# Kernel tuning notes

Measured on AMD Instinct MI355X. Metric: run time of the kernel, lower is better.

The kernel has to match this reference:

```python
import jax, jax.numpy as jnp
import numpy as np

B, S, D, H = 2, 2048, 1024, 16
DEPTH = D // H


def setup_inputs() -> dict:
    key = jax.random.key(0)
    ks = jax.random.split(key, 13)
    std = 1.0 / np.sqrt(D)
    inp = {
        'q': jax.random.normal(ks[0], (B, S, D), jnp.float32),
        'k': jax.random.normal(ks[1], (B, S, D), jnp.float32),
        'v': jax.random.normal(ks[2], (B, S, D), jnp.float32),
        # padding-style mask broadcastable to [B,H,Sq,Sk]; 1 = masked
        'mask': (jax.random.uniform(ks[3], (B, 1, 1, S)) < 0.1).astype(jnp.float32),
        'wq_w': jax.random.uniform(ks[4], (D, D), jnp.float32, -std, std),
        'wq_b': jax.random.uniform(ks[5], (D,), jnp.float32, -std, std),
        'wk_w': jax.random.uniform(ks[6], (D, D), jnp.float32, -std, std),
        'wk_b': jax.random.uniform(ks[7], (D,), jnp.float32, -std, std),
        'wv_w': jax.random.uniform(ks[8], (D, D), jnp.float32, -std, std),
        'wv_b': jax.random.uniform(ks[9], (D,), jnp.float32, -std, std),
        'wo_w': jax.random.uniform(ks[10], (D, D), jnp.float32, -std, std),
        'wo_b': jax.random.uniform(ks[11], (D,), jnp.float32, -std, std),
    }
    return inp


def _split_heads(x):
    # [B,S,D] -> [B,H,S,depth]
    b, s, _ = x.shape
    return x.reshape(b, s, H, DEPTH).transpose(0, 2, 1, 3)


def reference(q, k, v, mask, wq_w, wq_b, wk_w, wk_b, wv_w, wv_b, wo_w, wo_b):
    qh = _split_heads(q @ wq_w.T + wq_b)
    kh = _split_heads(k @ wk_w.T + wk_b)
    vh = _split_heads(v @ wv_w.T + wv_b)
    scale = 1.0 / jnp.sqrt(jnp.float32(DEPTH))
    logits = jnp.einsum('bhqd,bhkd->bhqk', qh, kh) * scale  # [B,H,S,S]
    logits = logits + mask * (-1e9)
    weights = jax.nn.softmax(logits, axis=-1)
    attn = jnp.einsum('bhqk,bhkd->bhqd', weights, vh)
    concat = attn.transpose(0, 2, 1, 3).reshape(q.shape[0], -1, D)
    out = concat @ wo_w.T + wo_b
    return out, weights
```

## Files before the change

### kernel.cpp

```cpp
#include <hip/hip_runtime.h>
#include <stdint.h>
#include <stddef.h>

static constexpr int NB = 2;
static constexpr int SS = 2048;
static constexpr int DDim = 1024;
static constexpr int NH = 16;
static constexpr size_t BSD = (size_t)NB * SS * DDim;
static constexpr size_t DDn = (size_t)DDim * DDim;

typedef __attribute__((ext_vector_type(4))) float f32x4;
typedef __attribute__((ext_vector_type(8))) short bf16x8;

__device__ __forceinline__ short f2bf(float f) {
  union { float f; unsigned u; } v; v.f = f;
  unsigned r = v.u + 0x7FFFu + ((v.u >> 16) & 1u);
  return (short)(r >> 16);
}

__device__ __forceinline__ void gload_lds16(const void* src, void* dst) {
  __builtin_amdgcn_global_load_lds(
      (const __attribute__((address_space(1))) void*)src,
      (__attribute__((address_space(3))) void*)dst, 16, 0, 0);
}

__global__ void cvt_k(const float* __restrict__ in, short* __restrict__ out, int n8) {
  int i = blockIdx.x * 256 + threadIdx.x;
  if (i >= n8) return;
  const f32x4* p = (const f32x4*)in + (size_t)i * 2;
  f32x4 a = p[0], c = p[1];
  bf16x8 o;
  o[0] = f2bf(a[0]); o[1] = f2bf(a[1]); o[2] = f2bf(a[2]); o[3] = f2bf(a[3]);
  o[4] = f2bf(c[0]); o[5] = f2bf(c[1]); o[6] = f2bf(c[2]); o[7] = f2bf(c[3]);
  ((bf16x8*)out)[i] = o;
}

__device__ __forceinline__ void gemm_core(
    const short* __restrict__ A, const short* __restrict__ Bm,
    int rowA, int rowB, int ld, int nk,
    short* la, short* lb, int wid, int lane, f32x4 (&acc)[4][4]) {
  const int ar = lane & 15, ak = (lane >> 4) * 8;
  const int srow = lane >> 2, scol = (lane & 3) * 8;
  const int wr = wid >> 1, wc = wid & 1;
  for (int kt = 0; kt < nk; ++kt) {
    const int k0 = kt * 32;
#pragma unroll
    for (int c = 0; c < 2; ++c) {
      int chunk = c * 4 + wid;
      gload_lds16(A + (size_t)(rowA + chunk * 16 + srow) * ld + k0 + scol, la + chunk * 512);
      gload_lds16(Bm + (size_t)(rowB + chunk * 16 + srow) * ld + k0 + scol, lb + chunk * 512);
    }
    asm volatile("s_waitcnt vmcnt(0)" ::: "memory");
    __syncthreads();
    bf16x8 af[4], bfr[4];
#pragma unroll
    for (int m = 0; m < 4; ++m)
      af[m] = *(const bf16x8*)(la + (wr * 64 + m * 16 + ar) * 32 + ak);
#pragma unroll
    for (int n = 0; n < 4; ++n)
      bfr[n] = *(const bf16x8*)(lb + (wc * 64 + n * 16 + ar) * 32 + ak);
#pragma unroll
    for (int m = 0; m < 4; ++m)
#pragma unroll
      for (int n = 0; n < 4; ++n)
        acc[m][n] = __builtin_amdgcn_mfma_f32_16x16x32_bf16(af[m], bfr[n], acc[m][n], 0, 0, 0);
    __syncthreads();
  }
}

template <int MODE>
__global__ __launch_bounds__(256, 2) void gemm128(
    const short* __restrict__ A, const short* __restrict__ Bm,
    const float* __restrict__ bias, void* __restrict__ outp, int N, int ld, int nk) {
  __shared__ short la[128 * 32], lb[128 * 32];
  const int tid = threadIdx.x, wid = tid >> 6, lane = tid & 63;
  const int bM = blockIdx.y * 128, bN = blockIdx.x * 128;
  f32x4 acc[4][4];
#pragma unroll
  for (int m = 0; m < 4; ++m)
#pragma unroll
    for (int n = 0; n < 4; ++n) acc[m][n] = (f32x4){0.f, 0.f, 0.f, 0.f};
  gemm_core(A, Bm, bM, bN, ld, nk, la, lb, wid, lane, acc);
  const int wr = wid >> 1, wc = wid & 1;
#pragma unroll
  for (int m = 0; m < 4; ++m)
#pragma unroll
    for (int n = 0; n < 4; ++n)
#pragma unroll
      for (int r = 0; r < 4; ++r) {
        int gm = bM + wr * 64 + m * 16 + (lane >> 4) * 4 + r;
        int gn = bN + wc * 64 + n * 16 + (lane & 15);
        float val = acc[m][n][r] + bias[gn];
        if constexpr (MODE == 0) {
          int b = gm >> 11, s = gm & 2047, h = gn >> 6, d = gn & 63;
          ((short*)outp)[(((size_t)b * NH + h) * SS + s) * 64 + d] = f2bf(val);
        } else if constexpr (MODE == 1) {
          int b = gm >> 11, s = gm & 2047, h = gn >> 6, d = gn & 63;
          ((short*)outp)[(((size_t)b * NH + h) * 64 + d) * SS + s] = f2bf(val);
        } else {
          ((float*)outp)[(size_t)gm * N + gn] = val;
        }
      }
}

__global__ __launch_bounds__(256, 2) void attn_k(
    const short* __restrict__ qh, const short* __restrict__ kh,
    const short* __restrict__ vhT, const float* __restrict__ mask,
    float* __restrict__ wout, short* __restrict__ concat) {
  __shared__ short lP[128 * 128];
  __shared__ short lK[128 * 64];
  __shared__ short lV[64 * 128];
  __shared__ float lmask[2048];
  __shared__ float lrs[2][128];
  const int tid = threadIdx.x, wid = tid >> 6, lane = tid & 63;
  const int wr = wid >> 1, wc = wid & 1;
  const int bh = blockIdx.y, b = bh >> 4, h = bh & 15;
  const int bM = blockIdx.x * 128;
  const short* Qb = qh + (size_t)bh * SS * 64 + (size_t)bM * 64;
  const short* Kb = kh + (size_t)bh * SS * 64;
  const short* Vb = vhT + (size_t)bh * 64 * SS;
  float* Wb = wout + (size_t)bh * SS * SS;

#pragma unroll
  for (int i = 0; i < 8; ++i)
    lmask[tid + i * 256] = mask[b * SS + tid + i * 256] * (-1e9f);

#pragma unroll
  for (int c = 0; c < 4; ++c) {
    int ob = c * 4096 + tid * 16;
    int row = ob >> 7, inrow = ob & 127;
    gload_lds16(Qb + row * 64 + ((inrow ^ ((row & 7) << 4)) >> 1), (char*)lP + ob);
  }
  asm volatile("s_waitcnt vmcnt(0)" ::: "memory");
  __syncthreads();
  bf16x8 af[4][2];
#pragma unroll
  for (int m = 0; m < 4; ++m)
#pragma unroll
    for (int kk = 0; kk < 2; ++kk) {
      int row = wr * 64 + m * 16 + (lane & 15);
      int kb = (kk * 32 + (lane >> 4) * 8) * 2;
      af[m][kk] = *(const bf16x8*)((const char*)lP + row * 128 + (kb ^ ((row & 7) << 4)));
    }

  float ps[4][4];
#pragma unroll
  for (int m = 0; m < 4; ++m)
#pragma unroll
    for (int r = 0; r < 4; ++r) ps[m][r] = 0.f;

  for (int kt = 0; kt < 16; ++kt) {
    __syncthreads();
#pragma unroll
    for (int c = 0; c < 4; ++c) {
      int ob = c * 4096 + tid * 16;
      int row = ob >> 7, inrow = ob & 127;
      gload_lds16(Kb + (size_t)(kt * 128 + row) * 64 + ((inrow ^ ((row & 7) << 4)) >> 1),
                  (char*)lK + ob);
    }
    asm volatile("s_waitcnt vmcnt(0)" ::: "memory");
    __syncthreads();
    bf16x8 bfr[4][2];
#pragma unroll
    for (int n = 0; n < 4; ++n)
#pragma unroll
      for (int kk = 0; kk < 2; ++kk) {
        int row = wc * 64 + n * 16 + (lane & 15);
        int kb = (kk * 32 + (lane >> 4) * 8) * 2;
        bfr[n][kk] = *(const bf16x8*)((const char*)lK + row * 128 + (kb ^ ((row & 7) << 4)));
      }
#pragma unroll
    for (int n = 0; n < 4; ++n) {
      float mv = lmask[kt * 128 + wc * 64 + n * 16 + (lane & 15)];
#pragma unroll
      for (int m = 0; m < 4; ++m) {
        f32x4 a = (f32x4){0.f, 0.f, 0.f, 0.f};
        a = __builtin_amdgcn_mfma_f32_16x16x32_bf16(af[m][0], bfr[n][0], a, 0, 0, 0);
        a = __builtin_amdgcn_mfma_f32_16x16x32_bf16(af[m][1], bfr[n][1], a, 0, 0, 0);
#pragma unroll
        for (int r = 0; r < 4; ++r) ps[m][r] += __expf(a[r] * 0.125f + mv);
      }
    }
  }
#pragma unroll
  for (int m = 0; m < 4; ++m)
#pragma unroll
    for (int r = 0; r < 4; ++r) {
      float s = ps[m][r];
      s += __shfl_xor(s, 1, 64);
      s += __shfl_xor(s, 2, 64);
      s += __shfl_xor(s, 4, 64);
      s += __shfl_xor(s, 8, 64);
      ps[m][r] = s;
    }
  if ((lane & 15) == 0) {
#pragma unroll
    for (int m = 0; m < 4; ++m)
#pragma unroll
      for (int r = 0; r < 4; ++r)
        lrs[wc][wr * 64 + m * 16 + (lane >> 4) * 4 + r] = ps[m][r];
  }
  __syncthreads();
  float inv[4][4];
#pragma unroll
  for (int m = 0; m < 4; ++m)
#pragma unroll
    for (int r = 0; r < 4; ++r) {
      int row = wr * 64 + m * 16 + (lane >> 4) * 4 + r;
      inv[m][r] = 1.f / (lrs[0][row] + lrs[1][row]);
    }

  f32x4 pacc[4][2];
#pragma unroll
  for (int m = 0; m < 4; ++m)
#pragma unroll
    for (int n = 0; n < 2; ++n) pacc[m][n] = (f32x4){0.f, 0.f, 0.f, 0.f};

  for (int kt = 0; kt < 16; ++kt) {
    __syncthreads();
#pragma unroll
    for (int c = 0; c < 4; ++c) {
      int ob = c * 4096 + tid * 16;
      int row = ob >> 7, inrow = ob & 127;
      gload_lds16(Kb + (size_t)(kt * 128 + row) * 64 + ((inrow ^ ((row & 7) << 4)) >> 1),
                  (char*)lK + ob);
    }
#pragma unroll
    for (int c = 0; c < 4; ++c) {
      int ob = c * 4096 + tid * 16;
      int row = ob >> 8, inrow = ob & 255;
      gload_lds16(Vb + (size_t)row * SS + kt * 128 + ((inrow ^ ((row & 7) << 4)) >> 1),
                  (char*)lV + ob);
    }
    asm volatile("s_waitcnt vmcnt(0)" ::: "memory");
    __syncthreads();
    bf16x8 bfr[4][2];
#pragma unroll
    for (int n = 0; n < 4; ++n)
#pragma unroll
      for (int kk = 0; kk < 2; ++kk) {
        int row = wc * 64 + n * 16 + (lane & 15);
        int kb = (kk * 32 + (lane >> 4) * 8) * 2;
        bfr[n][kk] = *(const bf16x8*)((const char*)lK + row * 128 + (kb ^ ((row & 7) << 4)));
      }
#pragma unroll
    for (int n = 0; n < 4; ++n) {
      int col = wc * 64 + n * 16 + (lane & 15);
      float mv = lmask[kt * 128 + col];
#pragma unroll
      for (int m = 0; m < 4; ++m) {
        f32x4 a = (f32x4){0.f, 0.f, 0.f, 0.f};
        a = __builtin_amdgcn_mfma_f32_16x16x32_bf16(af[m][0], bfr[n][0], a, 0, 0, 0);
        a = __builtin_amdgcn_mfma_f32_16x16x32_bf16(af[m][1], bfr[n][1], a, 0, 0, 0);
#pragma unroll
        for (int r = 0; r < 4; ++r) {
          int prow = wr * 64 + m * 16 + (lane >> 4) * 4 + r;
          float w = __expf(a[r] * 0.125f + mv) * inv[m][r];
          Wb[(size_t)(bM + prow) * SS + kt * 128 + col] = w;
          *(short*)((char*)lP + prow * 256 + ((col * 2) ^ ((prow & 7) << 4))) = f2bf(w);
        }
      }
    }
    __syncthreads();
#pragma unroll
    for (int kk = 0; kk < 4; ++kk) {
      bf16x8 pa[4], bv[2];
      int kb = (kk * 32 + (lane >> 4) * 8) * 2;
#pragma unroll
      for (int m = 0; m < 4; ++m) {
        int row = wr * 64 + m * 16 + (lane & 15);
        pa[m] = *(const bf16x8*)((const char*)lP + row * 256 + (kb ^ ((row & 7) << 4)));
      }
#pragma unroll
      for (int n = 0; n < 2; ++n) {
        int d = wc * 32 + n * 16 + (lane & 15);
        bv[n] = *(const bf16x8*)((const char*)lV + d * 256 + (kb ^ ((d & 7) << 4)));
      }
#pragma unroll
      for (int m = 0; m < 4; ++m)
#pragma unroll
        for (int n = 0; n < 2; ++n)
          pacc[m][n] = __builtin_amdgcn_mfma_f32_16x16x32_bf16(pa[m], bv[n], pacc[m][n], 0, 0, 0);
    }
  }
#pragma unroll
  for (int m = 0; m < 4; ++m)
#pragma unroll
    for (int n = 0; n < 2; ++n)
#pragma unroll
      for (int r = 0; r < 4; ++r) {
        int s = bM + wr * 64 + m * 16 + (lane >> 4) * 4 + r;
        int d = wc * 32 + n * 16 + (lane & 15);
        concat[((size_t)(b * SS + s)) * DDim + h * 64 + d] = f2bf(pacc[m][n][r]);
      }
}

extern "C" void kernel_launch(void* const* d_in, const int* in_sizes, int n_in,
                              void* d_out, int out_size, void* d_ws, size_t ws_size,
                              hipStream_t stream) {
  const float* q = (const float*)d_in[0];
  const float* k = (const float*)d_in[1];
  const float* v = (const float*)d_in[2];
  const float* mask = (const float*)d_in[3];
  const float* wq_w = (const float*)d_in[4];
  const float* wq_b = (const float*)d_in[5];
  const float* wk_w = (const float*)d_in[6];
  const float* wk_b = (const float*)d_in[7];
  const float* wv_w = (const float*)d_in[8];
  const float* wv_b = (const float*)d_in[9];
  const float* wo_w = (const float*)d_in[10];
  const float* wo_b = (const float*)d_in[11];

  short* qb = (short*)d_ws;
  short* kb = qb + BSD;
  short* vb = kb + BSD;
  short* wqb = vb + BSD;
  short* wkb = wqb + DDn;
  short* wvb = wkb + DDn;
  short* wob = wvb + DDn;
  short* qh = wob + DDn;
  short* kh = qh + BSD;
  short* vhT = kh + BSD;
  short* concat = vhT + BSD;

  float* out0 = (float*)d_out;
  float* wts = out0 + BSD;

  const int n8_bsd = (int)(BSD / 8), n8_dd = (int)(DDn / 8);
  cvt_k<<<n8_bsd / 256, 256, 0, stream>>>(q, qb, n8_bsd);
  cvt_k<<<n8_bsd / 256, 256, 0, stream>>>(k, kb, n8_bsd);
  cvt_k<<<n8_bsd / 256, 256, 0, stream>>>(v, vb, n8_bsd);
  cvt_k<<<n8_dd / 256, 256, 0, stream>>>(wq_w, wqb, n8_dd);
  cvt_k<<<n8_dd / 256, 256, 0, stream>>>(wk_w, wkb, n8_dd);
  cvt_k<<<n8_dd / 256, 256, 0, stream>>>(wv_w, wvb, n8_dd);
  cvt_k<<<n8_dd / 256, 256, 0, stream>>>(wo_w, wob, n8_dd);

  dim3 gproj(DDim / 128, (NB * SS) / 128);
  gemm128<0><<<gproj, 256, 0, stream>>>(qb, wqb, wq_b, qh, DDim, DDim, DDim / 32);
  gemm128<0><<<gproj, 256, 0, stream>>>(kb, wkb, wk_b, kh, DDim, DDim, DDim / 32);
  gemm128<1><<<gproj, 256, 0, stream>>>(vb, wvb, wv_b, vhT, DDim, DDim, DDim / 32);

  dim3 gattn(SS / 128, NB * NH);
  attn_k<<<gattn, 256, 0, stream>>>(qh, kh, vhT, mask, wts, concat);

  gemm128<2><<<gproj, 256, 0, stream>>>(concat, wob, wo_b, (void*)out0, DDim, DDim, DDim / 32);
}
```

Before: 331.4 us.

## Batch conversions and QKV projections into fewer launches with double-buffered GEMM

Merges the seven fp32-to-bf16 conversion launches into two and the three Q/K/V projection GEMMs into one launch with a z-dimension over projections. The GEMM main loop now double-buffers LDS tiles, so the next k-tile is issued before the current one's MFMAs and only one barrier is needed per iteration. The attention softmax switches from __expf to exp2f, with the log2(e) factor folded into the scale and mask constants. These changes target launch overhead, small-grid tail effects and load latency, at the cost of twice the LDS per GEMM block.

Result: faster. 315.5 us (-4.8%).

```diff
diff --git a/kernel.cpp b/kernel.cpp
--- a/kernel.cpp
+++ b/kernel.cpp
@@ -12,6 +12,9 @@
 typedef __attribute__((ext_vector_type(4))) float f32x4;
 typedef __attribute__((ext_vector_type(8))) short bf16x8;
 
+static constexpr float SCL2 = 0.125f * 1.4426950408889634f;
+static constexpr float MSK2 = -1.4426950408889634e9f;
+
 __device__ __forceinline__ short f2bf(float f) {
   union { float f; unsigned u; } v; v.f = f;
   unsigned r = v.u + 0x7FFFu + ((v.u >> 16) & 1u);
@@ -24,10 +27,13 @@
       (__attribute__((address_space(3))) void*)dst, 16, 0, 0);
 }
 
-__global__ void cvt_k(const float* __restrict__ in, short* __restrict__ out, int n8) {
+__global__ void cvtw_k(const float* __restrict__ w0, const float* __restrict__ w1,
+                       const float* __restrict__ w2, const float* __restrict__ w3,
+                       short* __restrict__ out) {
   int i = blockIdx.x * 256 + threadIdx.x;
-  if (i >= n8) return;
-  const f32x4* p = (const f32x4*)in + (size_t)i * 2;
+  int mat = i >> 17;
+  const float* src = mat == 0 ? w0 : mat == 1 ? w1 : mat == 2 ? w2 : w3;
+  const f32x4* p = (const f32x4*)src + (size_t)(i & 131071) * 2;
   f32x4 a = p[0], c = p[1];
   bf16x8 o;
   o[0] = f2bf(a[0]); o[1] = f2bf(a[1]); o[2] = f2bf(a[2]); o[3] = f2bf(a[3]);
@@ -35,53 +41,70 @@
   ((bf16x8*)out)[i] = o;
 }
 
-__device__ __forceinline__ void gemm_core(
-    const short* __restrict__ A, const short* __restrict__ Bm,
-    int rowA, int rowB, int ld, int nk,
-    short* la, short* lb, int wid, int lane, f32x4 (&acc)[4][4]) {
+__global__ void cvt3_k(const float* __restrict__ t0, const float* __restrict__ t1,
+                       const float* __restrict__ t2, short* __restrict__ out) {
+  int i = blockIdx.x * 256 + threadIdx.x;
+  int mat = i >> 19;
+  const float* src = mat == 0 ? t0 : mat == 1 ? t1 : t2;
+  const f32x4* p = (const f32x4*)src + (size_t)(i & 524287) * 2;
+  f32x4 a = p[0], c = p[1];
+  bf16x8 o;
+  o[0] = f2bf(a[0]); o[1] = f2bf(a[1]); o[2] = f2bf(a[2]); o[3] = f2bf(a[3]);
+  o[4] = f2bf(c[0]); o[5] = f2bf(c[1]); o[6] = f2bf(c[2]); o[7] = f2bf(c[3]);
+  ((bf16x8*)out)[i] = o;
+}
+
+__global__ __launch_bounds__(256, 2) void proj3_k(
+    const short* __restrict__ Acat, const short* __restrict__ Bcat,
+    const float* __restrict__ bq, const float* __restrict__ bk, const float* __restrict__ bv,
+    short* __restrict__ qh, short* __restrict__ kh, short* __restrict__ vhT) {
+  __shared__ short la[2][4096], lb[2][4096];
+  const int tid = threadIdx.x, wid = tid >> 6, lane = tid & 63;
+  const int proj = blockIdx.z;
+  const short* A = Acat + (size_t)proj * BSD;
+  const short* Bm = Bcat + (size_t)proj * DDn;
+  const float* bias = proj == 0 ? bq : proj == 1 ? bk : bv;
+  const int bM = blockIdx.y * 128, bN = blockIdx.x * 128;
   const int ar = lane & 15, ak = (lane >> 4) * 8;
   const int srow = lane >> 2, scol = (lane & 3) * 8;
   const int wr = wid >> 1, wc = wid & 1;
-  for (int kt = 0; kt < nk; ++kt) {
+  f32x4 acc[4][4];
+#pragma unroll
+  for (int m = 0; m < 4; ++m)
+#pragma unroll
+    for (int n = 0; n < 4; ++n) acc[m][n] = (f32x4){0.f, 0.f, 0.f, 0.f};
+
+  auto stage = [&](int kt, int bb) {
     const int k0 = kt * 32;
 #pragma unroll
     for (int c = 0; c < 2; ++c) {
       int chunk = c * 4 + wid;
-      gload_lds16(A + (size_t)(rowA + chunk * 16 + srow) * ld + k0 + scol, la + chunk * 512);
-      gload_lds16(Bm + (size_t)(rowB + chunk * 16 + srow) * ld + k0 + scol, lb + chunk * 512);
-    }
-    asm volatile("s_waitcnt vmcnt(0)" ::: "memory");
-    __syncthreads();
+      gload_lds16(A + (size_t)(bM + chunk * 16 + srow) * DDim + k0 + scol, &la[bb][chunk * 512]);
+      gload_lds16(Bm + (size_t)(bN + chunk * 16 + srow) * DDim + k0 + scol, &lb[bb][chunk * 512]);
+    }
+  };
+
+  stage(0, 0);
+  asm volatile("s_waitcnt vmcnt(0)" ::: "memory");
+  __syncthreads();
+  for (int kt = 0; kt < 32; ++kt) {
+    const int bb = kt & 1;
+    if (kt < 31) stage(kt + 1, bb ^ 1);
     bf16x8 af[4], bfr[4];
 #pragma unroll
     for (int m = 0; m < 4; ++m)
-      af[m] = *(const bf16x8*)(la + (wr * 64 + m * 16 + ar) * 32 + ak);
-#pragma unroll
-    for (int n = 0; n < 4; ++n)
-      bfr[n] = *(const bf16x8*)(lb + (wc * 64 + n * 16 + ar) * 32 + ak);
+      af[m] = *(const bf16x8*)(&la[bb][(wr * 64 + m * 16 + ar) * 32 + ak]);
+#pragma unroll
+    for (int n = 0; n < 4; ++n)
+      bfr[n] = *(const bf16x8*)(&lb[bb][(wc * 64 + n * 16 + ar) * 32 + ak]);
 #pragma unroll
     for (int m = 0; m < 4; ++m)
 #pragma unroll
       for (int n = 0; n < 4; ++n)
         acc[m][n] = __builtin_amdgcn_mfma_f32_16x16x32_bf16(af[m], bfr[n], acc[m][n], 0, 0, 0);
-    __syncthreads();
-  }
-}
-
-template <int MODE>
-__global__ __launch_bounds__(256, 2) void gemm128(
-    const short* __restrict__ A, const short* __restrict__ Bm,
-    const float* __restrict__ bias, void* __restrict__ outp, int N, int ld, int nk) {
-  __shared__ short la[128 * 32], lb[128 * 32];
-  const int tid = threadIdx.x, wid = tid >> 6, lane = tid & 63;
-  const int bM = blockIdx.y * 128, bN = blockIdx.x * 128;
-  f32x4 acc[4][4];
-#pragma unroll
-  for (int m = 0; m < 4; ++m)
-#pragma unroll
-    for (int n = 0; n < 4; ++n) acc[m][n] = (f32x4){0.f, 0.f, 0.f, 0.f};
-  gemm_core(A, Bm, bM, bN, ld, nk, la, lb, wid, lane, acc);
-  const int wr = wid >> 1, wc = wid & 1;
+    asm volatile("s_waitcnt vmcnt(0)" ::: "memory");
+    __syncthreads();
+  }
 #pragma unroll
   for (int m = 0; m < 4; ++m)
 #pragma unroll
@@ -91,15 +114,71 @@
         int gm = bM + wr * 64 + m * 16 + (lane >> 4) * 4 + r;
         int gn = bN + wc * 64 + n * 16 + (lane & 15);
         float val = acc[m][n][r] + bias[gn];
-        if constexpr (MODE == 0) {
-          int b = gm >> 11, s = gm & 2047, h = gn >> 6, d = gn & 63;
-          ((short*)outp)[(((size_t)b * NH + h) * SS + s) * 64 + d] = f2bf(val);
-        } else if constexpr (MODE == 1) {
-          int b = gm >> 11, s = gm & 2047, h = gn >> 6, d = gn & 63;
-          ((short*)outp)[(((size_t)b * NH + h) * 64 + d) * SS + s] = f2bf(val);
-        } else {
-          ((float*)outp)[(size_t)gm * N + gn] = val;
+        int b = gm >> 11, s = gm & 2047, h = gn >> 6, d = gn & 63;
+        if (proj == 2)
+          vhT[(((size_t)b * NH + h) * 64 + d) * SS + s] = f2bf(val);
+        else {
+          short* o = proj == 0 ? qh : kh;
+          o[(((size_t)b * NH + h) * SS + s) * 64 + d] = f2bf(val);
         }
+      }
+}
+
+__global__ __launch_bounds__(256, 2) void outproj_k(
+    const short* __restrict__ A, const short* __restrict__ Bm,
+    const float* __restrict__ bias, float* __restrict__ outp) {
+  __shared__ short la[2][4096], lb[2][4096];
+  const int tid = threadIdx.x, wid = tid >> 6, lane = tid & 63;
+  const int bM = blockIdx.y * 128, bN = blockIdx.x * 128;
+  const int ar = lane & 15, ak = (lane >> 4) * 8;
+  const int srow = lane >> 2, scol = (lane & 3) * 8;
+  const int wr = wid >> 1, wc = wid & 1;
+  f32x4 acc[4][4];
+#pragma unroll
+  for (int m = 0; m < 4; ++m)
+#pragma unroll
+    for (int n = 0; n < 4; ++n) acc[m][n] = (f32x4){0.f, 0.f, 0.f, 0.f};
+
+  auto stage = [&](int kt, int bb) {
+    const int k0 = kt * 32;
+#pragma unroll
+    for (int c = 0; c < 2; ++c) {
+      int chunk = c * 4 + wid;
+      gload_lds16(A + (size_t)(bM + chunk * 16 + srow) * DDim + k0 + scol, &la[bb][chunk * 512]);
+      gload_lds16(Bm + (size_t)(bN + chunk * 16 + srow) * DDim + k0 + scol, &lb[bb][chunk * 512]);
+    }
+  };
+
+  stage(0, 0);
+  asm volatile("s_waitcnt vmcnt(0)" ::: "memory");
+  __syncthreads();
+  for (int kt = 0; kt < 32; ++kt) {
+    const int bb = kt & 1;
+    if (kt < 31) stage(kt + 1, bb ^ 1);
+    bf16x8 af[4], bfr[4];
+#pragma unroll
+    for (int m = 0; m < 4; ++m)
+      af[m] = *(const bf16x8*)(&la[bb][(wr * 64 + m * 16 + ar) * 32 + ak]);
+#pragma unroll
+    for (int n = 0; n < 4; ++n)
+      bfr[n] = *(const bf16x8*)(&lb[bb][(wc * 64 + n * 16 + ar) * 32 + ak]);
+#pragma unroll
+    for (int m = 0; m < 4; ++m)
+#pragma unroll
+      for (int n = 0; n < 4; ++n)
+        acc[m][n] = __builtin_amdgcn_mfma_f32_16x16x32_bf16(af[m], bfr[n], acc[m][n], 0, 0, 0);
+    asm volatile("s_waitcnt vmcnt(0)" ::: "memory");
+    __syncthreads();
+  }
+#pragma unroll
+  for (int m = 0; m < 4; ++m)
+#pragma unroll
+    for (int n = 0; n < 4; ++n)
+#pragma unroll
+      for (int r = 0; r < 4; ++r) {
+        int gm = bM + wr * 64 + m * 16 + (lane >> 4) * 4 + r;
+        int gn = bN + wc * 64 + n * 16 + (lane & 15);
+        outp[(size_t)gm * DDim + gn] = acc[m][n][r] + bias[gn];
       }
 }
 
@@ -123,7 +202,7 @@
 
 #pragma unroll
   for (int i = 0; i < 8; ++i)
-    lmask[tid + i * 256] = mask[b * SS + tid + i * 256] * (-1e9f);
+    lmask[tid + i * 256] = mask[b * SS + tid + i * 256] * MSK2;
 
 #pragma unroll
   for (int c = 0; c < 4; ++c) {
@@ -178,7 +257,7 @@
         a = __builtin_amdgcn_mfma_f32_16x16x32_bf16(af[m][0], bfr[n][0], a, 0, 0, 0);
         a = __builtin_amdgcn_mfma_f32_16x16x32_bf16(af[m][1], bfr[n][1], a, 0, 0, 0);
 #pragma unroll
-        for (int r = 0; r < 4; ++r) ps[m][r] += __expf(a[r] * 0.125f + mv);
+        for (int r = 0; r < 4; ++r) ps[m][r] += exp2f(a[r] * SCL2 + mv);
       }
     }
   }
@@ -255,7 +334,7 @@
 #pragma unroll
         for (int r = 0; r < 4; ++r) {
           int prow = wr * 64 + m * 16 + (lane >> 4) * 4 + r;
-          float w = __expf(a[r] * 0.125f + mv) * inv[m][r];
+          float w = exp2f(a[r] * SCL2 + mv) * inv[m][r];
           Wb[(size_t)(bM + prow) * SS + kt * 128 + col] = w;
           *(short*)((char*)lP + prow * 256 + ((col * 2) ^ ((prow & 7) << 4))) = f2bf(w);
         }
@@ -312,12 +391,8 @@
   const float* wo_b = (const float*)d_in[11];
 
   short* qb = (short*)d_ws;
-  short* kb = qb + BSD;
-  short* vb = kb + BSD;
-  short* wqb = vb + BSD;
-  short* wkb = wqb + DDn;
-  short* wvb = wkb + DDn;
-  short* wob = wvb + DDn;
+  short* wqb = qb + 3 * BSD;
+  short* wob = wqb + 3 * DDn;
   short* qh = wob + DDn;
   short* kh = qh + BSD;
   short* vhT = kh + BSD;
@@ -326,22 +401,15 @@
   float* out0 = (float*)d_out;
   float* wts = out0 + BSD;
 
-  const int n8_bsd = (int)(BSD / 8), n8_dd = (int)(DDn / 8);
-  cvt_k<<<n8_bsd / 256, 256, 0, stream>>>(q, qb, n8_bsd);
-  cvt_k<<<n8_bsd / 256, 256, 0, stream>>>(k, kb, n8_bsd);
-  cvt_k<<<n8_bsd / 256, 256, 0, stream>>>(v, vb, n8_bsd);
-  cvt_k<<<n8_dd / 256, 256, 0, stream>>>(wq_w, wqb, n8_dd);
-  cvt_k<<<n8_dd / 256, 256, 0, stream>>>(wk_w, wkb, n8_dd);
-  cvt_k<<<n8_dd / 256, 256, 0, stream>>>(wv_w, wvb, n8_dd);
-  cvt_k<<<n8_dd / 256, 256, 0, stream>>>(wo_w, wob, n8_dd);
-
-  dim3 gproj(DDim / 128, (NB * SS) / 128);
-  gemm128<0><<<gproj, 256, 0, stream>>>(qb, wqb, wq_b, qh, DDim, DDim, DDim / 32);
-  gemm128<0><<<gproj, 256, 0, stream>>>(kb, wkb, wk_b, kh, DDim, DDim, DDim / 32);
-  gemm128<1><<<gproj, 256, 0, stream>>>(vb, wvb, wv_b, vhT, DDim, DDim, DDim / 32);
+  cvtw_k<<<2048, 256, 0, stream>>>(wq_w, wk_w, wv_w, wo_w, wqb);
+  cvt3_k<<<6144, 256, 0, stream>>>(q, k, v, qb);
+
+  dim3 gproj(DDim / 128, (NB * SS) / 128, 3);
+  proj3_k<<<gproj, 256, 0, stream>>>(qb, wqb, wq_b, wk_b, wv_b, qh, kh, vhT);
 
   dim3 gattn(SS / 128, NB * NH);
   attn_k<<<gattn, 256, 0, stream>>>(qh, kh, vhT, mask, wts, concat);
 
-  gemm128<2><<<gproj, 256, 0, stream>>>(concat, wob, wo_b, (void*)out0, DDim, DDim, DDim / 32);
-}
+  dim3 gout(DDim / 128, (NB * SS) / 128);
+  outproj_k<<<gout, 256, 0, stream>>>(concat, wob, wo_b, out0);
+}
```
